# Kernel tuning notes

Measured on AMD Instinct MI355X. Metric: run time of the kernel, lower is better.

Reference implementation:

```python
import jax, jax.numpy as jnp
import numpy as np

HID = 2048      # hidden_size
NH = 16         # num_attention_heads
QLR = 1536      # q_lora_rank
KVLR = 512      # kv_lora_rank
DN = 128        # qk_nope_head_dim
DR = 64         # qk_rope_head_dim
DQK = DN + DR   # qk_head_dim = 192
DV = 128        # v_head_dim
EPS = 1e-6
THETA = 10000.0
B, T = 2, 2048


def rmsnorm(x, scale):
    return x * jax.lax.rsqrt(jnp.mean(x * x, axis=-1, keepdims=True) + EPS) * scale


def rope(x, positions):
    # x: [B, T, h, d]; NeoX-style rotate-half RoPE on the rope slice only
    d = x.shape[-1]
    inv_freq = 1.0 / (THETA ** (jnp.arange(0, d, 2, dtype=jnp.float32) / d))
    ang = positions.astype(jnp.float32)[..., None] * inv_freq       # [B, T, d/2]
    cos = jnp.cos(ang)[:, :, None, :]
    sin = jnp.sin(ang)[:, :, None, :]
    x1, x2 = jnp.split(x, 2, axis=-1)
    return jnp.concatenate([x1 * cos - x2 * sin, x2 * cos + x1 * sin], axis=-1).astype(x.dtype)


def setup_inputs() -> dict:
    key = jax.random.key(0)
    ks = jax.random.split(key, 8)
    s = 0.02
    x = jax.random.normal(ks[0], (B, T, HID), dtype=jnp.float32)
    attention_mask = jnp.ones((B, T), dtype=bool)
    positions = jnp.broadcast_to(jnp.arange(T, dtype=jnp.int32), (B, T))
    wqa = jax.random.normal(ks[1], (HID, QLR), dtype=jnp.float32) * s
    qa_scale = jnp.ones((QLR,), dtype=jnp.float32)
    wqb = jax.random.normal(ks[2], (QLR, NH * DQK), dtype=jnp.float32) * s
    wkva = jax.random.normal(ks[3], (HID, KVLR + DR), dtype=jnp.float32) * s
    kva_scale = jnp.ones((KVLR,), dtype=jnp.float32)
    wkvb = jax.random.normal(ks[4], (KVLR, NH * (DN + DV)), dtype=jnp.float32) * s
    wo = jax.random.normal(ks[5], (NH * DV, HID), dtype=jnp.float32) * s
    return {"x": x, "attention_mask": attention_mask, "positions": positions,
            "wqa": wqa, "qa_scale": qa_scale, "wqb": wqb,
            "wkva": wkva, "kva_scale": kva_scale, "wkvb": wkvb, "wo": wo}


def reference(x, attention_mask, positions, wqa, qa_scale, wqb, wkva, kva_scale, wkvb, wo):
    Bv, Tv, _ = x.shape
    # low-rank Q: hid -> q_lora_rank -> rmsnorm -> heads*qk_head_dim
    q = (rmsnorm(x @ wqa, qa_scale) @ wqb).reshape(Bv, Tv, NH, DQK)
    q_pass, q_rot = q[..., :DN], q[..., DN:]
    # compressed KV + shared rope key
    ckv = x @ wkva                                    # [B, T, KVLR + DR]
    kv_lat, k_rot = ckv[..., :KVLR], ckv[..., KVLR:].reshape(Bv, Tv, 1, DR)
    kv = (rmsnorm(kv_lat, kva_scale) @ wkvb).reshape(Bv, Tv, NH, DN + DV)
    k_pass, v = kv[..., :DN], kv[..., DN:]
    # decoupled RoPE on rope slice only
    q_rot = rope(q_rot, positions)
    k_rot = jnp.broadcast_to(rope(k_rot, positions), (Bv, Tv, NH, DR))
    q = jnp.concatenate([q_pass, q_rot], axis=-1)     # [B, T, H, 192]
    k = jnp.concatenate([k_pass, k_rot], axis=-1)
    # masked causal SDPA; v padding in the original is a no-op mathematically
    scale = DQK ** -0.5
    scores = jnp.einsum('bqhd,bkhd->bhqk', q, k) * scale
    causal = jnp.tril(jnp.ones((Tv, Tv), dtype=bool))
    mask = causal[None, None, :, :] & attention_mask[:, None, None, :].astype(bool)
    scores = jnp.where(mask, scores, jnp.finfo(scores.dtype).min)
    probs = jax.nn.softmax(scores, axis=-1)
    out = jnp.einsum('bhqk,bkhd->bqhd', probs, v).reshape(Bv, Tv, NH * DV)
    return out @ wo
```

## Files before the change

kernel.cpp:

```cpp
#include <hip/hip_runtime.h>
#include <math.h>
#include <stdint.h>

#define NHEAD 16
#define HIDDIM 2048
#define QLRANK 1536
#define KVRANK 512
#define DROT 64
#define BB 2
#define TT 2048
#define BTOK (BB*TT)
#define NPROJ 2176
#define CKV0 1536
#define ROT0 2048

typedef __bf16 bf16x8 __attribute__((ext_vector_type(8)));
typedef __bf16 bf16x4 __attribute__((ext_vector_type(4)));
typedef float f32x4 __attribute__((ext_vector_type(4)));
typedef uint16_t u16;
typedef uint32_t u32;

__device__ __forceinline__ u16 f2bf(float f) {
  union { float f; uint32_t u; } v; v.f = f;
  uint32_t r = v.u + 0x7fffu + ((v.u >> 16) & 1u);
  return (u16)(r >> 16);
}
__device__ __forceinline__ float bf2f(u16 h) {
  union { uint32_t u; float f; } v; v.u = ((uint32_t)h) << 16;
  return v.f;
}

__device__ __forceinline__ void gload_lds16(const u16* g, u16* l) {
  __builtin_amdgcn_global_load_lds(
      (const __attribute__((address_space(1))) uint32_t*)g,
      (__attribute__((address_space(3))) uint32_t*)l, 16, 0, 0);
}

__global__ __launch_bounds__(256) void cvt_f32_bf16(const float* __restrict__ in,
                                                    u16* __restrict__ out, int n) {
  int idx = (blockIdx.x * 256 + threadIdx.x) * 8;
  if (idx >= n) return;
  f32x4 a = *(const f32x4*)&in[idx];
  f32x4 b = *(const f32x4*)&in[idx + 4];
  union { f32x4 q; u16 e[8]; } w;
#pragma unroll
  for (int j = 0; j < 4; ++j) { w.e[j] = f2bf(a[j]); w.e[4 + j] = f2bf(b[j]); }
  *(f32x4*)&out[idx] = w.q;
}

__global__ __launch_bounds__(256) void transpose_w(const float* __restrict__ W,
                                                   u16* __restrict__ Wt,
                                                   int K, int N, int Npad, float scale,
                                                   const float* __restrict__ svec) {
  __shared__ float tile[32][33];
  int k0 = blockIdx.x * 32, n0 = blockIdx.y * 32;
  int tx = threadIdx.x, ty = threadIdx.y;
#pragma unroll
  for (int r = 0; r < 32; r += 8) {
    int k = k0 + ty + r, n = n0 + tx;
    tile[ty + r][tx] = (k < K && n < N) ? W[(size_t)k * N + n] : 0.f;
  }
  __syncthreads();
  float sv = scale * (svec ? svec[k0 + tx] : 1.f);
#pragma unroll
  for (int r = 0; r < 32; r += 8) {
    int n = n0 + ty + r, k = k0 + tx;
    if (n < Npad && k < K) Wt[(size_t)n * K + k] = f2bf(tile[tx][ty + r] * sv);
  }
}

template<int D>
__global__ __launch_bounds__(256) void row_invrms(const u16* __restrict__ in, int stride,
                                                  float* __restrict__ out) {
  const int row = blockIdx.x;
  const int tid = threadIdx.x;
  constexpr int NC = D / 8;
  float ss = 0.f;
  if (tid < NC) {
    union { f32x4 q; u16 e[8]; } t;
    t.q = *(const f32x4*)&in[(size_t)row * stride + tid * 8];
#pragma unroll
    for (int j = 0; j < 8; ++j) { float v = bf2f(t.e[j]); ss += v * v; }
  }
#pragma unroll
  for (int off = 1; off < 64; off <<= 1) ss += __shfl_xor(ss, off);
  __shared__ float red[4];
  if ((tid & 63) == 0) red[tid >> 6] = ss;
  __syncthreads();
  if (tid == 0)
    out[row] = rsqrtf((red[0] + red[1] + red[2] + red[3]) / (float)D + 1e-6f);
}

template<int OUTF32>
__global__ __launch_bounds__(256) void gemm_bt(const u16* __restrict__ A, int lda,
                                               const u16* __restrict__ Bt,
                                               void* __restrict__ Cv, int ldc,
                                               const float* __restrict__ rowscale,
                                               int N, int K) {
  __shared__ __align__(16) u16 As[2][128 * 32];
  __shared__ __align__(16) u16 Bs[2][128 * 32];
  const int tid = threadIdx.x;
  const int lane = tid & 63;
  const int wave = tid >> 6;
  const int bm = blockIdx.y * 128;
  const int bn = blockIdx.x * 128;
  const int wr = wave >> 1;
  const int wc = wave & 1;

  f32x4 acc[4][4] = {};

  const int srow = wave * 16 + (lane >> 2);
  const int scol = (lane & 3) * 8;
  const u16* Ag = A + (size_t)(bm + srow) * lda + scol;
  const u16* Bg = Bt + (size_t)(bn + srow) * K + scol;
  const int soff = (wave * 16) * 32;

  const int a_off = (wr * 64 + (lane & 15)) * 32 + (lane >> 4) * 8;
  const int b_off = (wc * 64 + (lane & 15)) * 32 + (lane >> 4) * 8;

  const int nt = K >> 5;

  gload_lds16(Ag, &As[0][soff]);
  gload_lds16(Ag + (size_t)64 * lda, &As[0][soff + 64 * 32]);
  gload_lds16(Bg, &Bs[0][soff]);
  gload_lds16(Bg + (size_t)64 * K, &Bs[0][soff + 64 * 32]);
  __syncthreads();

  int cur = 0;
  for (int t = 0; t < nt; ++t) {
    if (t + 1 < nt) {
      const int k0 = (t + 1) << 5;
      gload_lds16(Ag + k0, &As[cur ^ 1][soff]);
      gload_lds16(Ag + (size_t)64 * lda + k0, &As[cur ^ 1][soff + 64 * 32]);
      gload_lds16(Bg + k0, &Bs[cur ^ 1][soff]);
      gload_lds16(Bg + (size_t)64 * K + k0, &Bs[cur ^ 1][soff + 64 * 32]);
    }
    bf16x8 af[4], bfr[4];
#pragma unroll
    for (int m = 0; m < 4; ++m) af[m] = *(const bf16x8*)&As[cur][a_off + m * 16 * 32];
#pragma unroll
    for (int n = 0; n < 4; ++n) bfr[n] = *(const bf16x8*)&Bs[cur][b_off + n * 16 * 32];
#pragma unroll
    for (int m = 0; m < 4; ++m)
#pragma unroll
      for (int n = 0; n < 4; ++n)
        acc[m][n] = __builtin_amdgcn_mfma_f32_16x16x32_bf16(af[m], bfr[n], acc[m][n], 0, 0, 0);
    if (t + 1 < nt) {
      __syncthreads();
      cur ^= 1;
    }
  }

  const int row0 = bm + wr * 64 + (lane >> 4) * 4;
  const int col0 = bn + wc * 64 + (lane & 15);
#pragma unroll
  for (int m = 0; m < 4; ++m) {
    float rs[4] = {1.f, 1.f, 1.f, 1.f};
    if (rowscale) {
#pragma unroll
      for (int i = 0; i < 4; ++i) rs[i] = rowscale[row0 + m * 16 + i];
    }
#pragma unroll
    for (int n = 0; n < 4; ++n)
#pragma unroll
      for (int i = 0; i < 4; ++i) {
        size_t idx = (size_t)(row0 + m * 16 + i) * ldc + (col0 + n * 16);
        float v = acc[m][n][i] * rs[i];
        if (OUTF32) ((float*)Cv)[idx] = v;
        else        ((u16*)Cv)[idx] = f2bf(v);
      }
  }
}

__global__ __launch_bounds__(256) void rope_table(const int* __restrict__ positions,
                                                  float2* __restrict__ tab) {
  int idx = blockIdx.x * 256 + threadIdx.x;
  if (idx >= BTOK * 32) return;
  int bt = idx >> 5, i = idx & 31;
  float invf = powf(10000.0f, -(float)i / 32.0f);
  float ang = (float)positions[bt] * invf;
  tab[idx] = make_float2(cosf(ang), sinf(ang));
}

__global__ __launch_bounds__(256) void rope_q(u16* __restrict__ q,
                                              const float2* __restrict__ tab) {
  int idx = blockIdx.x * 256 + threadIdx.x;
  if (idx >= BTOK * NHEAD * 32) return;
  int i = idx & 31;
  int h = (idx >> 5) & 15;
  int bt = idx >> 9;
  u16* p = q + (size_t)bt * 3072 + h * 192 + 128;
  float x1 = bf2f(p[i]), x2 = bf2f(p[32 + i]);
  float2 cs = tab[bt * 32 + i];
  p[i] = f2bf(x1 * cs.x - x2 * cs.y);
  p[32 + i] = f2bf(x2 * cs.x + x1 * cs.y);
}

__global__ __launch_bounds__(256) void assemble_k(const u16* __restrict__ kv,
                                                  const u16* __restrict__ proj,
                                                  const float2* __restrict__ tab,
                                                  u16* __restrict__ kf) {
  int bt = blockIdx.x;
  __shared__ __align__(16) u16 krot[64];
  int t = threadIdx.x;
  if (t < 64) {
    int i = t & 31;
    float2 cs = tab[bt * 32 + i];
    float x1 = bf2f(proj[(size_t)bt * NPROJ + ROT0 + i]);
    float x2 = bf2f(proj[(size_t)bt * NPROJ + ROT0 + 32 + i]);
    krot[t] = f2bf((t < 32) ? (x1 * cs.x - x2 * cs.y) : (x2 * cs.x + x1 * cs.y));
  }
  __syncthreads();
  for (int c = t; c < 16 * 24; c += 256) {
    int h = c / 24, seg = c % 24;
    u16* dst = kf + (size_t)bt * 3072 + h * 192 + seg * 8;
    if (seg < 16)
      *(f32x4*)dst = *(const f32x4*)&kv[(size_t)bt * 4096 + h * 256 + seg * 8];
    else
      *(f32x4*)dst = *(const f32x4*)&krot[(seg - 16) * 8];
  }
}

__device__ const int8_t JOB_QT[24] = {15,15,7,14,14,13,13,6,12,12,11,11,5,10,10,9,9,4,8,8,3,2,1,0};
__device__ const int8_t JOB_PC[24] = { 0, 1,2, 0, 1, 0, 1,2, 0, 1, 0, 1,2, 0, 1,0,1,2,0,1,2,2,2,2};

__global__ __launch_bounds__(256, 2) void attn_fwd4(const u16* __restrict__ Q,
                                                    const u16* __restrict__ Kf,
                                                    const u16* __restrict__ KV,
                                                    u16* __restrict__ O,
                                                    u16* __restrict__ Opart,
                                                    float2* __restrict__ ml) {
  __shared__ __align__(16) u16 Ks[64 * 192];
  __shared__ __align__(16) u16 Vs[64 * 128];

  const int tid = threadIdx.x, lane = tid & 63, wave = tid >> 6;
  const int l15 = lane & 15, l4 = lane >> 4;
  const int jobrank = blockIdx.x >> 5;
  const int bh = blockIdx.x & 31;
  const int qt = JOB_QT[jobrank];
  const int piece = JOB_PC[jobrank];
  const int q0 = qt * 128;
  const int b = bh >> 4, h = bh & 15;
  const int wq0 = q0 + wave * 32;

  bf16x8 qf[2][6];
#pragma unroll
  for (int m = 0; m < 2; ++m) {
    const u16* qp = Q + (size_t)(b * TT + wq0 + m * 16 + l15) * 3072 + h * 192 + l4 * 8;
#pragma unroll
    for (int kk = 0; kk < 6; ++kk) qf[m][kk] = *(const bf16x8*)(qp + kk * 32);
  }

  int ksrc[6];
#pragma unroll
  for (int j = 0; j < 6; ++j) {
    int o = (wave * 6 + j) * 1024 + lane * 16;
    int row = o / 384, col = o % 384;
    int scol = col ^ ((row & 7) << 4);
    ksrc[j] = row * 3072 + (scol >> 1);
  }
  int vsrc[4];
#pragma unroll
  for (int j = 0; j < 4; ++j) {
    int lam = (wave * 4 + j) * 512 + lane * 8;
    int kap = ((lam >> 6) & 15) * 4 + ((lam >> 4) & 3);
    int key = ((kap >> 5) & 1) * 32 + ((kap >> 2) & 3) * 8 + ((kap >> 4) & 1) * 4 + (kap & 3);
    int dv  = (lam >> 10) * 16 + (lam & 15);
    vsrc[j] = key * 4096 + dv;
  }
  const u16* Kbase = Kf + (size_t)(b * TT) * 3072 + h * 192;
  const u16* Vbase = KV + (size_t)(b * TT) * 4096 + h * 256 + 128;
  u16* KsW = Ks + (wave * 6) * 512;
  u16* VsW = Vs + (wave * 4) * 512;
  const unsigned vs_base = (unsigned)(uintptr_t)(&Vs[0]);

  f32x4 o_acc[2][8] = {};
  float m_r[2], l_r[2];
#pragma unroll
  for (int m = 0; m < 2; ++m) { m_r[m] = -INFINITY; l_r[m] = 0.f; }

  const int kt0 = (piece == 1) ? (qt + 1) : 0;
  const int kt1 = (piece == 0) ? (qt + 1) : (2 * qt + 2);

  for (int kt = kt0; kt < kt1; ++kt) {
    __syncthreads();
    const u16* Kt = Kbase + (size_t)(kt * 64) * 3072;
    const u16* Vt = Vbase + (size_t)(kt * 64) * 4096;
#pragma unroll
    for (int j = 0; j < 6; ++j) gload_lds16(Kt + ksrc[j], KsW + j * 512);
#pragma unroll
    for (int j = 0; j < 4; ++j) gload_lds16(Vt + vsrc[j], VsW + j * 512);
    __syncthreads();

    if (kt * 64 > wq0 + 31) continue;
    const int kt64 = kt * 64;

    f32x4 s[2][4] = {};
    __builtin_amdgcn_s_setprio(1);
#pragma unroll
    for (int n = 0; n < 4; ++n) {
      const int krow = n * 16 + l15;
      const int swz = (l15 & 7) << 3;
#pragma unroll
      for (int kk = 0; kk < 6; ++kk) {
        bf16x8 kb = *(const bf16x8*)&Ks[krow * 192 + ((kk * 32 + l4 * 8) ^ swz)];
        s[0][n] = __builtin_amdgcn_mfma_f32_16x16x32_bf16(kb, qf[0][kk], s[0][n], 0, 0, 0);
        s[1][n] = __builtin_amdgcn_mfma_f32_16x16x32_bf16(kb, qf[1][kk], s[1][n], 0, 0, 0);
      }
    }
    __builtin_amdgcn_s_setprio(0);

    u32 pk[2][4][2];
#pragma unroll
    for (int m = 0; m < 2; ++m) {
      const int qrow = wq0 + m * 16 + l15;
      const bool needmask = (kt64 + 63) > (wq0 + m * 16);
      if (needmask) {
#pragma unroll
        for (int n = 0; n < 4; ++n)
#pragma unroll
          for (int i = 0; i < 4; ++i)
            if (kt64 + n * 16 + l4 * 4 + i > qrow) s[m][n][i] = -INFINITY;
      }
      float pmax = -INFINITY;
#pragma unroll
      for (int n = 0; n < 4; ++n)
#pragma unroll
        for (int i = 0; i < 4; ++i) pmax = fmaxf(pmax, s[m][n][i]);
      pmax = fmaxf(pmax, __shfl_xor(pmax, 16));
      pmax = fmaxf(pmax, __shfl_xor(pmax, 32));

      if (!__all(pmax - m_r[m] <= 8.f)) {
        float mn = fmaxf(m_r[m], pmax);
        float alpha = __expf(m_r[m] - mn);
        m_r[m] = mn;
        l_r[m] *= alpha;
        float ab[4];
#pragma unroll
        for (int i = 0; i < 4; ++i) ab[i] = __shfl(alpha, l4 * 4 + i);
#pragma unroll
        for (int n = 0; n < 8; ++n)
#pragma unroll
          for (int i = 0; i < 4; ++i) o_acc[m][n][i] *= ab[i];
      }

      float psum = 0.f;
#pragma unroll
      for (int n = 0; n < 4; ++n) {
        float p0 = __expf(s[m][n][0] - m_r[m]);
        float p1 = __expf(s[m][n][1] - m_r[m]);
        float p2 = __expf(s[m][n][2] - m_r[m]);
        float p3 = __expf(s[m][n][3] - m_r[m]);
        psum += (p0 + p1) + (p2 + p3);
        union { u32 u; __bf16 e[2]; } a, c;
        a.e[0] = (__bf16)p0; a.e[1] = (__bf16)p1;
        c.e[0] = (__bf16)p2; c.e[1] = (__bf16)p3;
        pk[m][n][0] = a.u;
        pk[m][n][1] = c.u;
      }
      psum += __shfl_xor(psum, 16);
      psum += __shfl_xor(psum, 32);
      l_r[m] += psum;
    }

#pragma unroll
    for (int kk = 0; kk < 2; ++kk) {
      bf16x8 pa[2];
#pragma unroll
      for (int m = 0; m < 2; ++m) {
        union { u32 w[4]; bf16x8 v; } uu;
#pragma unroll
        for (int t = 0; t < 4; ++t) {
          int src = l15 + ((2 * (l4 & 1) + (t >> 1)) << 4);
          u32 a0 = __shfl(pk[m][2 * kk + 0][t & 1], src);
          u32 a1 = __shfl(pk[m][2 * kk + 1][t & 1], src);
          uu.w[t] = (l4 & 2) ? a1 : a0;
        }
        pa[m] = uu.v;
      }
      const unsigned va = vs_base + kk * 1024 + lane * 8;
#pragma unroll
      for (int g = 0; g < 2; ++g) {
        union { uint2 u; bf16x4 b; } lo[4], hi[4];
#pragma unroll
        for (int n = 0; n < 4; ++n) {
          unsigned a0 = va + (g * 4 + n) * 2048;
          asm volatile("ds_read_b64_tr_b16 %0, %1" : "=v"(lo[n].u) : "v"(a0));
          asm volatile("ds_read_b64_tr_b16 %0, %1 offset:512" : "=v"(hi[n].u) : "v"(a0));
        }
        asm volatile("s_waitcnt lgkmcnt(0)" ::: "memory");
        __builtin_amdgcn_sched_barrier(0);
        __builtin_amdgcn_s_setprio(1);
#pragma unroll
        for (int n = 0; n < 4; ++n) {
          bf16x8 vb = __builtin_shufflevector(lo[n].b, hi[n].b, 0, 1, 2, 3, 4, 5, 6, 7);
          o_acc[0][g * 4 + n] = __builtin_amdgcn_mfma_f32_16x16x32_bf16(pa[0], vb, o_acc[0][g * 4 + n], 0, 0, 0);
          o_acc[1][g * 4 + n] = __builtin_amdgcn_mfma_f32_16x16x32_bf16(pa[1], vb, o_acc[1][g * 4 + n], 0, 0, 0);
        }
        __builtin_amdgcn_s_setprio(0);
      }
    }
  }

  if (piece == 2) {
#pragma unroll
    for (int m = 0; m < 2; ++m) {
      float inv = 1.f / l_r[m];
      float li[4];
#pragma unroll
      for (int i = 0; i < 4; ++i) li[i] = __shfl(inv, l4 * 4 + i);
#pragma unroll
      for (int n = 0; n < 8; ++n)
#pragma unroll
        for (int i = 0; i < 4; ++i) {
          int r = wq0 + m * 16 + l4 * 4 + i;
          O[(size_t)(b * TT + r) * 2048 + h * 128 + n * 16 + l15] = f2bf(o_acc[m][n][i] * li[i]);
        }
    }
  } else {
    const size_t pidx = ((size_t)(qt - 8) * 32 + bh) * 2 + piece;
    u16* op = Opart + pidx * (128 * 128);
    float2* mlp = ml + pidx * 128;
#pragma unroll
    for (int m = 0; m < 2; ++m)
#pragma unroll
      for (int n = 0; n < 8; ++n)
#pragma unroll
        for (int i = 0; i < 4; ++i)
          op[(wave * 32 + m * 16 + l4 * 4 + i) * 128 + n * 16 + l15] = f2bf(o_acc[m][n][i]);
    if (l4 == 0) {
#pragma unroll
      for (int m = 0; m < 2; ++m)
        mlp[wave * 32 + m * 16 + l15] = make_float2(m_r[m], l_r[m]);
    }
  }
}

__global__ __launch_bounds__(256) void attn_combine(const u16* __restrict__ Opart,
                                                    const float2* __restrict__ ml,
                                                    u16* __restrict__ O) {
  int gid = blockIdx.x * 256 + threadIdx.x;
  int dvseg = gid & 15;
  int row = (gid >> 4) & 127;
  int bh = (gid >> 11) & 31;
  int qt8 = gid >> 16;
  size_t i1 = ((size_t)qt8 * 32 + bh) * 2;
  float2 ml1 = ml[i1 * 128 + row], ml2 = ml[(i1 + 1) * 128 + row];
  float m = fmaxf(ml1.x, ml2.x);
  float w1 = __expf(ml1.x - m), w2 = __expf(ml2.x - m);
  float inv = 1.f / (w1 * ml1.y + w2 * ml2.y);
  union { f32x4 q; u16 e[8]; } a, bq, w;
  a.q  = *(const f32x4*)&Opart[i1 * 16384 + row * 128 + dvseg * 8];
  bq.q = *(const f32x4*)&Opart[(i1 + 1) * 16384 + row * 128 + dvseg * 8];
#pragma unroll
  for (int j = 0; j < 8; ++j)
    w.e[j] = f2bf((w1 * bf2f(a.e[j]) + w2 * bf2f(bq.e[j])) * inv);
  int b = bh >> 4, h = bh & 15;
  int r = 1024 + qt8 * 128 + row;
  *(f32x4*)&O[(size_t)(b * TT + r) * 2048 + h * 128 + dvseg * 8] = w.q;
}

extern "C" void kernel_launch(void* const* d_in, const int* in_sizes, int n_in,
                              void* d_out, int out_size, void* d_ws, size_t ws_size,
                              hipStream_t stream) {
  (void)in_sizes; (void)n_in; (void)out_size; (void)ws_size;
  const float* x         = (const float*)d_in[0];
  const int*   positions = (const int*)d_in[2];
  const float* wqa       = (const float*)d_in[3];
  const float* qa_scale  = (const float*)d_in[4];
  const float* wqb       = (const float*)d_in[5];
  const float* wkva      = (const float*)d_in[6];
  const float* kva_scale = (const float*)d_in[7];
  const float* wkvb      = (const float*)d_in[8];
  const float* wo        = (const float*)d_in[9];
  float* out = (float*)d_out;

  char* wsp = (char*)d_ws;
  auto alloc = [&](size_t bytes) {
    char* p = wsp; wsp += (bytes + 255) & ~(size_t)255; return p;
  };
  u16* xb      = (u16*)alloc((size_t)BTOK * HIDDIM * 2);
  u16* proj_t  = (u16*)alloc((size_t)NPROJ * HIDDIM * 2);
  u16* wqb_t   = (u16*)alloc((size_t)3072 * QLRANK * 2);
  u16* wkvb_t  = (u16*)alloc((size_t)4096 * KVRANK * 2);
  u16* wo_t    = (u16*)alloc((size_t)HIDDIM * HIDDIM * 2);
  u16* proj    = (u16*)alloc((size_t)BTOK * NPROJ * 2);
  u16* q       = (u16*)alloc((size_t)BTOK * 3072 * 2);
  u16* kv      = (u16*)alloc((size_t)BTOK * 4096 * 2);
  u16* kf      = (u16*)alloc((size_t)BTOK * 3072 * 2);
  float2* tab  = (float2*)alloc((size_t)BTOK * 32 * 8);
  float* invq  = (float*)alloc((size_t)BTOK * 4);
  float* invkv = (float*)alloc((size_t)BTOK * 4);
  float2* mlbuf= (float2*)alloc((size_t)8 * 32 * 2 * 128 * 8);
  u16* ao = xb;
  u16* Opart = proj;

  dim3 blk(256);
  const float qscale = 0.07216878364870322f;

  cvt_f32_bf16<<<(BTOK * HIDDIM / 8 + 255) / 256, blk, 0, stream>>>(x, xb, BTOK * HIDDIM);
  {
    dim3 tb(32, 8);
    transpose_w<<<dim3(HIDDIM / 32, QLRANK / 32), tb, 0, stream>>>(wqa, proj_t, HIDDIM, QLRANK, QLRANK, 1.f, nullptr);
    transpose_w<<<dim3(HIDDIM / 32, (NPROJ - CKV0) / 32), tb, 0, stream>>>(wkva, proj_t + (size_t)CKV0 * HIDDIM, HIDDIM, 576, NPROJ - CKV0, 1.f, nullptr);
    transpose_w<<<dim3(QLRANK / 32, 3072 / 32), tb, 0, stream>>>(wqb, wqb_t, QLRANK, 3072, 3072, qscale, qa_scale);
    transpose_w<<<dim3(KVRANK / 32, 4096 / 32), tb, 0, stream>>>(wkvb, wkvb_t, KVRANK, 4096, 4096, 1.f, kva_scale);
    transpose_w<<<dim3(HIDDIM / 32, HIDDIM / 32), tb, 0, stream>>>(wo, wo_t, HIDDIM, HIDDIM, HIDDIM, 1.f, nullptr);
  }
  rope_table<<<(BTOK * 32 + 255) / 256, blk, 0, stream>>>(positions, tab);

  gemm_bt<0><<<dim3(NPROJ / 128, BTOK / 128), blk, 0, stream>>>(xb, HIDDIM, proj_t, proj, NPROJ, nullptr, NPROJ, HIDDIM);

  row_invrms<QLRANK><<<BTOK, blk, 0, stream>>>(proj, NPROJ, invq);
  row_invrms<KVRANK><<<BTOK, blk, 0, stream>>>(proj + CKV0, NPROJ, invkv);

  gemm_bt<0><<<dim3(3072 / 128, BTOK / 128), blk, 0, stream>>>(proj, NPROJ, wqb_t, q, 3072, invq, 3072, QLRANK);
  gemm_bt<0><<<dim3(4096 / 128, BTOK / 128), blk, 0, stream>>>(proj + CKV0, NPROJ, wkvb_t, kv, 4096, invkv, 4096, KVRANK);

  rope_q<<<(BTOK * NHEAD * 32 + 255) / 256, blk, 0, stream>>>(q, tab);
  assemble_k<<<BTOK, blk, 0, stream>>>(kv, proj, tab, kf);

  attn_fwd4<<<dim3(24 * 32), blk, 0, stream>>>(q, kf, kv, ao, Opart, mlbuf);
  attn_combine<<<(8 * 32 * 128 * 16) / 256, blk, 0, stream>>>(Opart, mlbuf, ao);

  gemm_bt<1><<<dim3(HIDDIM / 128, BTOK / 128), blk, 0, stream>>>(ao, HIDDIM, wo_t, out, HIDDIM, nullptr, HIDDIM, HIDDIM);
}
```

Measured before the change: 347.9 us.

## Replace 128x128 GEMM with 256x256 tile, 512-thread, swizzled LDS pipelined kernel

Replaces the 128x128x32 double-buffered GEMM with a 256x256x64 tile kernel using 8 waves, XOR-swizzled LDS layout, explicit vmcnt waits, barriers and MFMA priority hints. NPROJ is padded to 2304 so the fused projection width divides by 256. The larger tile raises arithmetic intensity per LDS/global byte, but it uses 128KB of LDS and yields fewer blocks (e.g. 128 for the wo GEMM and 144 for the projection GEMM), which may underfill the 256 CUs.

```diff
diff --git a/kernel.cpp b/kernel.cpp
--- a/kernel.cpp
+++ b/kernel.cpp
@@ -10,7 +10,7 @@
 #define BB 2
 #define TT 2048
 #define BTOK (BB*TT)
-#define NPROJ 2176
+#define NPROJ 2304
 #define CKV0 1536
 #define ROT0 2048
 
@@ -92,80 +92,112 @@
 }
 
 template<int OUTF32>
-__global__ __launch_bounds__(256) void gemm_bt(const u16* __restrict__ A, int lda,
-                                               const u16* __restrict__ Bt,
-                                               void* __restrict__ Cv, int ldc,
-                                               const float* __restrict__ rowscale,
-                                               int N, int K) {
-  __shared__ __align__(16) u16 As[2][128 * 32];
-  __shared__ __align__(16) u16 Bs[2][128 * 32];
-  const int tid = threadIdx.x;
-  const int lane = tid & 63;
-  const int wave = tid >> 6;
-  const int bm = blockIdx.y * 128;
-  const int bn = blockIdx.x * 128;
-  const int wr = wave >> 1;
-  const int wc = wave & 1;
-
-  f32x4 acc[4][4] = {};
-
-  const int srow = wave * 16 + (lane >> 2);
-  const int scol = (lane & 3) * 8;
-  const u16* Ag = A + (size_t)(bm + srow) * lda + scol;
-  const u16* Bg = Bt + (size_t)(bn + srow) * K + scol;
-  const int soff = (wave * 16) * 32;
-
-  const int a_off = (wr * 64 + (lane & 15)) * 32 + (lane >> 4) * 8;
-  const int b_off = (wc * 64 + (lane & 15)) * 32 + (lane >> 4) * 8;
-
-  const int nt = K >> 5;
-
-  gload_lds16(Ag, &As[0][soff]);
-  gload_lds16(Ag + (size_t)64 * lda, &As[0][soff + 64 * 32]);
-  gload_lds16(Bg, &Bs[0][soff]);
-  gload_lds16(Bg + (size_t)64 * K, &Bs[0][soff + 64 * 32]);
-  __syncthreads();
-
-  int cur = 0;
+__global__ __launch_bounds__(512, 2) void gemm256(const u16* __restrict__ A, int lda,
+                                                  const u16* __restrict__ Bt,
+                                                  void* __restrict__ Cv, int ldc,
+                                                  const float* __restrict__ rowscale,
+                                                  int K) {
+  __shared__ __align__(16) u16 S[2][2][16384];
+  const int tid = threadIdx.x, lane = tid & 63, wave = tid >> 6;
+  const int l15 = lane & 15, l4 = lane >> 4;
+  const int bm = blockIdx.y * 256, bn = blockIdx.x * 256;
+  const int wm = wave >> 2, wn = wave & 3;
+
+  const int rlo = lane >> 3;
+  const int cbase = ((lane & 7) * 8) ^ ((lane >> 5) << 4);
+  const u16* src[8];
+  u16* dst[8];
+#pragma unroll
+  for (int j = 0; j < 8; ++j) {
+    int gj = wave * 8 + j;
+    if (gj < 32) {
+      src[j] = A + (size_t)(bm + gj * 8 + rlo) * lda + cbase;
+      dst[j] = &S[0][0][0] + gj * 512;
+    } else {
+      src[j] = Bt + (size_t)(bn + (gj - 32) * 8 + rlo) * K + cbase;
+      dst[j] = &S[0][1][0] + (gj - 32) * 512;
+    }
+  }
+
+  const int flip = ((l15 >> 2) & 1) << 5;
+  const char* Sa0 = (const char*)&S[0][0][0] + wm * 16384;
+  const char* Sb0 = (const char*)&S[0][1][0] + (wn >> 1) * 16384;
+  const int arow0 = l15 * 128 + l4 * 16;
+  const int brow0 = ((wn & 1) * 64 + l15) * 128 + l4 * 16;
+
+  f32x4 acc[8][4] = {};
+  const int nt = K >> 6;
+
+#pragma unroll
+  for (int j = 0; j < 8; ++j) gload_lds16(src[j], dst[j]);
+#pragma unroll
+  for (int j = 0; j < 8; ++j) gload_lds16(src[j] + 64, dst[j] + 32768);
+  asm volatile("s_waitcnt vmcnt(8)" ::: "memory");
+  __builtin_amdgcn_s_barrier();
+  __builtin_amdgcn_sched_barrier(0);
+
   for (int t = 0; t < nt; ++t) {
+    const char* Sab = Sa0 + (t & 1) * 65536;
+    const char* Sbb = Sb0 + (t & 1) * 65536;
+    bf16x8 bfr[4][2];
+#pragma unroll
+    for (int fn = 0; fn < 4; ++fn) {
+      bfr[fn][0] = *(const bf16x8*)(Sbb + ((brow0 + fn * 2048) ^ flip));
+      bfr[fn][1] = *(const bf16x8*)(Sbb + ((brow0 + fn * 2048 + 64) ^ flip));
+    }
+#pragma unroll
+    for (int q = 0; q < 4; ++q) {
+      bf16x8 a0[2], a1[2];
+#pragma unroll
+      for (int m2 = 0; m2 < 2; ++m2) {
+        const int fm = q * 2 + m2;
+        bf16x8 x0 = *(const bf16x8*)(Sab + ((arow0 + fm * 2048) ^ flip));
+        bf16x8 x1 = *(const bf16x8*)(Sab + ((arow0 + fm * 2048 + 64) ^ flip));
+        a0[m2] = x0; a1[m2] = x1;
+      }
+      __builtin_amdgcn_s_setprio(1);
+#pragma unroll
+      for (int m2 = 0; m2 < 2; ++m2)
+#pragma unroll
+        for (int fn = 0; fn < 4; ++fn) {
+          f32x4 c = acc[q * 2 + m2][fn];
+          c = __builtin_amdgcn_mfma_f32_16x16x32_bf16(a0[m2], bfr[fn][0], c, 0, 0, 0);
+          c = __builtin_amdgcn_mfma_f32_16x16x32_bf16(a1[m2], bfr[fn][1], c, 0, 0, 0);
+          acc[q * 2 + m2][fn] = c;
+        }
+      __builtin_amdgcn_s_setprio(0);
+    }
     if (t + 1 < nt) {
-      const int k0 = (t + 1) << 5;
-      gload_lds16(Ag + k0, &As[cur ^ 1][soff]);
-      gload_lds16(Ag + (size_t)64 * lda + k0, &As[cur ^ 1][soff + 64 * 32]);
-      gload_lds16(Bg + k0, &Bs[cur ^ 1][soff]);
-      gload_lds16(Bg + (size_t)64 * K + k0, &Bs[cur ^ 1][soff + 64 * 32]);
-    }
-    bf16x8 af[4], bfr[4];
-#pragma unroll
-    for (int m = 0; m < 4; ++m) af[m] = *(const bf16x8*)&As[cur][a_off + m * 16 * 32];
-#pragma unroll
-    for (int n = 0; n < 4; ++n) bfr[n] = *(const bf16x8*)&Bs[cur][b_off + n * 16 * 32];
-#pragma unroll
-    for (int m = 0; m < 4; ++m)
-#pragma unroll
-      for (int n = 0; n < 4; ++n)
-        acc[m][n] = __builtin_amdgcn_mfma_f32_16x16x32_bf16(af[m], bfr[n], acc[m][n], 0, 0, 0);
-    if (t + 1 < nt) {
-      __syncthreads();
-      cur ^= 1;
-    }
-  }
-
-  const int row0 = bm + wr * 64 + (lane >> 4) * 4;
-  const int col0 = bn + wc * 64 + (lane & 15);
-#pragma unroll
-  for (int m = 0; m < 4; ++m) {
+      __builtin_amdgcn_s_barrier();
+      __builtin_amdgcn_sched_barrier(0);
+      if (t + 2 < nt) {
+        const int koff = (t + 2) * 64;
+#pragma unroll
+        for (int j = 0; j < 8; ++j) gload_lds16(src[j] + koff, dst[j] + (t & 1) * 32768);
+        asm volatile("s_waitcnt vmcnt(8)" ::: "memory");
+      } else {
+        asm volatile("s_waitcnt vmcnt(0)" ::: "memory");
+      }
+      __builtin_amdgcn_s_barrier();
+      __builtin_amdgcn_sched_barrier(0);
+    }
+  }
+
+  const int row0 = bm + wm * 128 + l4 * 4;
+  const int col0 = bn + wn * 64 + l15;
+#pragma unroll
+  for (int fm = 0; fm < 8; ++fm) {
     float rs[4] = {1.f, 1.f, 1.f, 1.f};
     if (rowscale) {
 #pragma unroll
-      for (int i = 0; i < 4; ++i) rs[i] = rowscale[row0 + m * 16 + i];
-    }
-#pragma unroll
-    for (int n = 0; n < 4; ++n)
+      for (int i = 0; i < 4; ++i) rs[i] = rowscale[row0 + fm * 16 + i];
+    }
+#pragma unroll
+    for (int fn = 0; fn < 4; ++fn)
 #pragma unroll
       for (int i = 0; i < 4; ++i) {
-        size_t idx = (size_t)(row0 + m * 16 + i) * ldc + (col0 + n * 16);
-        float v = acc[m][n][i] * rs[i];
+        size_t idx = (size_t)(row0 + fm * 16 + i) * ldc + (col0 + fn * 16);
+        float v = acc[fm][fn][i] * rs[i];
         if (OUTF32) ((float*)Cv)[idx] = v;
         else        ((u16*)Cv)[idx] = f2bf(v);
       }
@@ -496,6 +528,7 @@
   u16* Opart = proj;
 
   dim3 blk(256);
+  dim3 blk512(512);
   const float qscale = 0.07216878364870322f;
 
   cvt_f32_bf16<<<(BTOK * HIDDIM / 8 + 255) / 256, blk, 0, stream>>>(x, xb, BTOK * HIDDIM);
@@ -509,13 +542,13 @@
   }
   rope_table<<<(BTOK * 32 + 255) / 256, blk, 0, stream>>>(positions, tab);
 
-  gemm_bt<0><<<dim3(NPROJ / 128, BTOK / 128), blk, 0, stream>>>(xb, HIDDIM, proj_t, proj, NPROJ, nullptr, NPROJ, HIDDIM);
+  gemm256<0><<<dim3(NPROJ / 256, BTOK / 256), blk512, 0, stream>>>(xb, HIDDIM, proj_t, proj, NPROJ, nullptr, HIDDIM);
 
   row_invrms<QLRANK><<<BTOK, blk, 0, stream>>>(proj, NPROJ, invq);
   row_invrms<KVRANK><<<BTOK, blk, 0, stream>>>(proj + CKV0, NPROJ, invkv);
 
-  gemm_bt<0><<<dim3(3072 / 128, BTOK / 128), blk, 0, stream>>>(proj, NPROJ, wqb_t, q, 3072, invq, 3072, QLRANK);
-  gemm_bt<0><<<dim3(4096 / 128, BTOK / 128), blk, 0, stream>>>(proj + CKV0, NPROJ, wkvb_t, kv, 4096, invkv, 4096, KVRANK);
+  gemm256<0><<<dim3(3072 / 256, BTOK / 256), blk512, 0, stream>>>(proj, NPROJ, wqb_t, q, 3072, invq, QLRANK);
+  gemm256<0><<<dim3(4096 / 256, BTOK / 256), blk512, 0, stream>>>(proj + CKV0, NPROJ, wkvb_t, kv, 4096, invkv, KVRANK);
 
   rope_q<<<(BTOK * NHEAD * 32 + 255) / 256, blk, 0, stream>>>(q, tab);
   assemble_k<<<BTOK, blk, 0, stream>>>(kv, proj, tab, kf);
@@ -523,5 +556,5 @@
   attn_fwd4<<<dim3(24 * 32), blk, 0, stream>>>(q, kf, kv, ao, Opart, mlbuf);
   attn_combine<<<(8 * 32 * 128 * 16) / 256, blk, 0, stream>>>(Opart, mlbuf, ao);
 
-  gemm_bt<1><<<dim3(HIDDIM / 128, BTOK / 128), blk, 0, stream>>>(ao, HIDDIM, wo_t, out, HIDDIM, nullptr, HIDDIM, HIDDIM);
-}
+  gemm256<1><<<dim3(HIDDIM / 256, BTOK / 256), blk512, 0, stream>>>(ao, HIDDIM, wo_t, out, HIDDIM, nullptr, HIDDIM);
+}
```

Measured after the change: 374.6 us. +7.7%, slower.
